# Optimization experiments

Measured on AMD Instinct MI355X. Metric: run time of the kernel, lower is better.

The kernel has to match this reference:

```python
import jax, jax.numpy as jnp
import numpy as np

TARGET_W, TARGET_H = 1024, 1024  # cv2 target_size = (width, height)
LANCZOS_A = 4  # cv2.INTER_LANCZOS4 -> 8-tap separable Lanczos, a=4


def _lanczos_matrix(n_in: int, n_out: int) -> jnp.ndarray:
    """Dense [n_out, n_in] separable Lanczos4 resampling matrix.

    OpenCV pixel-center mapping: src = (dst + 0.5) * (n_in / n_out) - 0.5,
    8 taps around floor(src), weights normalized to sum 1, replicate border.
    """
    a = LANCZOS_A
    scale = n_in / n_out
    centers = (jnp.arange(n_out, dtype=jnp.float32) + 0.5) * scale - 0.5
    base = jnp.floor(centers).astype(jnp.int32)
    taps = jnp.arange(-a + 1, a + 1, dtype=jnp.int32)          # [-3..4], 8 taps
    idx = base[:, None] + taps[None, :]                         # [n_out, 8]
    d = centers[:, None] - idx.astype(jnp.float32)
    w = jnp.sinc(d) * jnp.sinc(d / a)                           # lanczos(d)
    w = jnp.where(jnp.abs(d) < a, w, 0.0)
    w = w / jnp.sum(w, axis=1, keepdims=True)
    idx_c = jnp.clip(idx, 0, n_in - 1)                          # replicate border
    rows = jnp.broadcast_to(jnp.arange(n_out)[:, None], idx.shape)
    return jnp.zeros((n_out, n_in), dtype=jnp.float32).at[rows, idx_c].add(w)


def _resize_lanczos4(x: jnp.ndarray, out_h: int, out_w: int) -> jnp.ndarray:
    # x: [B, C, H, W] -> [B, C, out_h, out_w] via two GEMM contractions
    Wh = _lanczos_matrix(x.shape[2], out_h)
    Ww = _lanczos_matrix(x.shape[3], out_w)
    t = jnp.einsum('oh,bchw->bcow', Wh, x)   # resample height: o=out_h
    return jnp.einsum('pw,bcow->bcop', Ww, t)  # resample width: p=out_w


def _renormalize(img: jnp.ndarray) -> jnp.ndarray:
    # Per-image (over C,H,W) range renormalization, faithful to the torch loop.
    mn = jnp.min(img, axis=(1, 2, 3), keepdims=True)
    mx = jnp.max(img, axis=(1, 2, 3), keepdims=True)
    color_range = mx - mn
    ott = jnp.float32(1.0 / 255.0)    # over_top_target_range
    ubt = jnp.float32(-10.0 / 255.0)  # under_bottom_target_range
    otr = mx - 1.0                    # over_top_range
    safe_otr = jnp.where(otr != 0, otr, 1.0)
    v1 = jnp.where(img > 1,
                   (img - 1.0) * (ott / safe_otr) + (1.0 - ott),
                   jnp.where(img < 1, img * (1.0 - ott), img))
    safe_ubr = jnp.where(mn != 0, mn, 1.0)  # under_bottom_range = mn (pre-modification)
    v2 = jnp.where(v1 < 0,
                   v1 * (ubt / safe_ubr) + ubt,
                   jnp.where(v1 > 0, v1 * (1.0 - ubt), v1))
    return jnp.where(color_range > 1, v2, img)


def setup_inputs() -> dict:
    key = jax.random.key(0)
    x = jax.random.normal(key, (32, 3, 512, 512), dtype=jnp.float32)
    return {"x": x}


def reference(x):
    y = _resize_lanczos4(x, TARGET_H, TARGET_W)
    y = _renormalize(y)
    y = y * 255.0
    return y.astype(jnp.uint8)
```

## Files before the change

kernel.cpp:

```cpp
#include <hip/hip_runtime.h>

#define IN_HW 512
#define OUT_HW 1024
#define NB 32
#define NC 3
#define TOH 32
#define TOW 128
#define PATCH_H 24
#define PATCH_W 72
#define NTHREADS 256

__device__ __forceinline__ unsigned enc_f(float f) {
  unsigned u = __float_as_uint(f);
  return (u & 0x80000000u) ? ~u : (u | 0x80000000u);
}
__device__ __forceinline__ float dec_f(unsigned k) {
  unsigned u = (k & 0x80000000u) ? (k ^ 0x80000000u) : ~k;
  return __uint_as_float(u);
}

#define LW_A -0.00397053f
#define LW_B  0.03146474f
#define LW_C -0.09165979f
#define LW_D  0.28268104f
#define LW_E  0.89337959f
#define LW_F -0.15228947f
#define LW_G  0.05544842f
#define LW_H -0.01505400f

__global__ void k_init(unsigned* __restrict__ maxk, unsigned* __restrict__ mink) {
  int i = threadIdx.x;
  if (i < NB) maxk[i] = 0u;
  else if (i < 2 * NB) mink[i - NB] = 0xFFFFFFFFu;
}

__global__ __launch_bounds__(NTHREADS) void k_resize(
    const float* __restrict__ x, float* __restrict__ outf,
    unsigned* __restrict__ maxk, unsigned* __restrict__ mink) {
  __shared__ __align__(16) float patch[PATCH_H][PATCH_W];
  __shared__ float wred[8];
  const int tid = threadIdx.x;
  const int bc = blockIdx.z;
  const int oh0 = blockIdx.y * TOH, ow0 = blockIdx.x * TOW;
  const int row0 = (oh0 >> 1) - 4;
  const int col0 = (ow0 >> 1) - 4;
  const float* __restrict__ xchan = x + (size_t)bc * (IN_HW * IN_HW);

  const bool interior = (row0 >= 0) & (row0 + PATCH_H <= IN_HW) &
                        (col0 >= 0) & (col0 + PATCH_W <= IN_HW);
  if (interior) {
    for (int e = tid; e < PATCH_H * (PATCH_W / 4); e += NTHREADS) {
      int pr = e / (PATCH_W / 4), pc4 = e - pr * (PATCH_W / 4);
      const float4 v = *reinterpret_cast<const float4*>(
          xchan + (size_t)(row0 + pr) * IN_HW + (col0 + 4 * pc4));
      *reinterpret_cast<float4*>(&patch[pr][4 * pc4]) = v;
    }
  } else {
    for (int e = tid; e < PATCH_H * PATCH_W; e += NTHREADS) {
      int pr = e / PATCH_W, pc = e - pr * PATCH_W;
      int gr = row0 + pr; gr = gr < 0 ? 0 : (gr > IN_HW - 1 ? IN_HW - 1 : gr);
      int gc = col0 + pc; gc = gc < 0 ? 0 : (gc > IN_HW - 1 ? IN_HW - 1 : gc);
      patch[pr][pc] = xchan[(size_t)gr * IN_HW + gc];
    }
  }
  __syncthreads();

  const int o = tid & 15;
  const int p = tid >> 4;

  const float w0[8] = {LW_A, LW_B, LW_C, LW_D, LW_E, LW_F, LW_G, LW_H};
  const float w1[8] = {LW_H, LW_G, LW_F, LW_E, LW_D, LW_C, LW_B, LW_A};

  float ve[12], vo[12];
#pragma unroll
  for (int c = 0; c < 12; ++c) { ve[c] = 0.f; vo[c] = 0.f; }
#pragma unroll
  for (int j = 0; j < 9; ++j) {
#pragma unroll
    for (int g = 0; g < 3; ++g) {
      const float4 t = *reinterpret_cast<const float4*>(&patch[p + j][4 * (o + g)]);
      const float tv[4] = {t.x, t.y, t.z, t.w};
#pragma unroll
      for (int c = 0; c < 4; ++c) {
        if (j < 8) ve[4 * g + c] = fmaf(w0[j], tv[c], ve[4 * g + c]);
        if (j > 0) vo[4 * g + c] = fmaf(w1[j - 1], tv[c], vo[4 * g + c]);
      }
    }
  }

  float mx = -__builtin_inff(), mn = __builtin_inff();
  const size_t base = (size_t)bc * (OUT_HW * OUT_HW) +
                      (size_t)(oh0 + 2 * p) * OUT_HW + (ow0 + 8 * o);
#pragma unroll
  for (int row = 0; row < 2; ++row) {
    const float* v = row ? vo : ve;
    float px[8];
#pragma unroll
    for (int m = 0; m < 4; ++m) {
      float pe = 0.f, po = 0.f;
#pragma unroll
      for (int j = 0; j < 8; ++j) {
        pe = fmaf(w0[j], v[m + j], pe);
        po = fmaf(w1[j], v[m + 1 + j], po);
      }
      px[2 * m] = pe; px[2 * m + 1] = po;
    }
#pragma unroll
    for (int i = 0; i < 8; ++i) { mx = fmaxf(mx, px[i]); mn = fminf(mn, px[i]); }
    float* dst = outf + base + (size_t)row * OUT_HW;
    *reinterpret_cast<float4*>(dst)     = make_float4(px[0], px[1], px[2], px[3]);
    *reinterpret_cast<float4*>(dst + 4) = make_float4(px[4], px[5], px[6], px[7]);
  }

#pragma unroll
  for (int s = 32; s > 0; s >>= 1) {
    mx = fmaxf(mx, __shfl_xor(mx, s, 64));
    mn = fminf(mn, __shfl_xor(mn, s, 64));
  }
  if ((tid & 63) == 0) { wred[tid >> 6] = mx; wred[4 + (tid >> 6)] = mn; }
  __syncthreads();
  if (tid == 0) {
    float bmx = fmaxf(fmaxf(wred[0], wred[1]), fmaxf(wred[2], wred[3]));
    float bmn = fminf(fminf(wred[4], wred[5]), fminf(wred[6], wred[7]));
    int b = bc / NC;
    atomicMax(&maxk[b], enc_f(bmx));
    atomicMin(&mink[b], enc_f(bmn));
  }
}

__device__ __forceinline__ int renorm1(float img, bool applies, float cA, float cB,
                                       float om_ott, float om_ubt) {
  const float ott = 1.0f / 255.0f;
  const float ubt = -10.0f / 255.0f;
  float v1 = (img > 1.0f) ? fmaf(img - 1.0f, cA, 1.0f - ott)
           : (img < 1.0f) ? img * om_ott : img;
  float v2 = (v1 < 0.0f) ? fmaf(v1, cB, ubt)
           : (v1 > 0.0f) ? v1 * om_ubt : v1;
  float y = (applies ? v2 : img) * 255.0f;
  int t = (int)y;
  return t < 0 ? 0 : (t > 255 ? 255 : t);
}

#define N4_PER_IMG (NC * OUT_HW * OUT_HW / 4)

__global__ __launch_bounds__(NTHREADS) void k_renorm(
    int* out, const unsigned* __restrict__ maxk, const unsigned* __restrict__ mink) {
  const int b = blockIdx.y;
  const float mx = dec_f(maxk[b]);
  const float mn = dec_f(mink[b]);
  const bool applies = (mx - mn) > 1.0f;
  const float ott = 1.0f / 255.0f;
  const float ubt = -10.0f / 255.0f;
  const float otr = mx - 1.0f;
  const float cA = ott / ((otr != 0.0f) ? otr : 1.0f);
  const float cB = ubt / ((mn != 0.0f) ? mn : 1.0f);
  const float om_ott = 1.0f - ott;
  const float om_ubt = 1.0f - ubt;

  const size_t idx = (size_t)b * N4_PER_IMG +
                     (size_t)blockIdx.x * NTHREADS + threadIdx.x;
  const float4 v = reinterpret_cast<const float4*>(out)[idx];
  int4 r;
  r.x = renorm1(v.x, applies, cA, cB, om_ott, om_ubt);
  r.y = renorm1(v.y, applies, cA, cB, om_ott, om_ubt);
  r.z = renorm1(v.z, applies, cA, cB, om_ott, om_ubt);
  r.w = renorm1(v.w, applies, cA, cB, om_ott, om_ubt);
  reinterpret_cast<int4*>(out)[idx] = r;
}

extern "C" void kernel_launch(void* const* d_in, const int* in_sizes, int n_in,
                              void* d_out, int out_size, void* d_ws, size_t ws_size,
                              hipStream_t stream) {
  const float* x = (const float*)d_in[0];
  unsigned* maxk = (unsigned*)d_ws;
  unsigned* mink = maxk + NB;

  hipLaunchKernelGGL(k_init, dim3(1), dim3(64), 0, stream, maxk, mink);
  dim3 grid(OUT_HW / TOW, OUT_HW / TOH, NB * NC);
  hipLaunchKernelGGL(k_resize, grid, dim3(NTHREADS), 0, stream,
                     x, (float*)d_out, maxk, mink);
  hipLaunchKernelGGL(k_renorm, dim3(N4_PER_IMG / NTHREADS, NB), dim3(NTHREADS),
                     0, stream, (int*)d_out, maxk, mink);
}
```

Measured before the change: 815.3 us.

## Recompute Lanczos resize in two passes instead of materializing float intermediate

Splits the pipeline into a min/max pass that runs the separable Lanczos resize and only reduces per-image extrema, and a final pass that recomputes the resize and applies renormalization and quantization directly before storing. This removes the full-size float intermediate write and its read-back, at the cost of reading the input and doing the resize arithmetic twice. The shared-memory patch row is also padded from 72 to 76 floats, likely to change LDS bank mapping; this also makes the interior fast path apply to fewer tiles.

After: 855.4 us. 1.05x slower.

```diff
diff --git a/kernel.cpp b/kernel.cpp
--- a/kernel.cpp
+++ b/kernel.cpp
@@ -7,7 +7,8 @@
 #define TOH 32
 #define TOW 128
 #define PATCH_H 24
-#define PATCH_W 72
+#define PATCH_W 76
+#define PATCH_QW (PATCH_W / 4)
 #define NTHREADS 256
 
 __device__ __forceinline__ unsigned enc_f(float f) {
@@ -34,23 +35,16 @@
   else if (i < 2 * NB) mink[i - NB] = 0xFFFFFFFFu;
 }
 
-__global__ __launch_bounds__(NTHREADS) void k_resize(
-    const float* __restrict__ x, float* __restrict__ outf,
-    unsigned* __restrict__ maxk, unsigned* __restrict__ mink) {
-  __shared__ __align__(16) float patch[PATCH_H][PATCH_W];
-  __shared__ float wred[8];
-  const int tid = threadIdx.x;
-  const int bc = blockIdx.z;
-  const int oh0 = blockIdx.y * TOH, ow0 = blockIdx.x * TOW;
+__device__ __forceinline__ void lanczos_tile(
+    const float* __restrict__ xchan, int oh0, int ow0, int tid,
+    float (*patch)[PATCH_W], float pr2[2][8]) {
   const int row0 = (oh0 >> 1) - 4;
   const int col0 = (ow0 >> 1) - 4;
-  const float* __restrict__ xchan = x + (size_t)bc * (IN_HW * IN_HW);
-
   const bool interior = (row0 >= 0) & (row0 + PATCH_H <= IN_HW) &
                         (col0 >= 0) & (col0 + PATCH_W <= IN_HW);
   if (interior) {
-    for (int e = tid; e < PATCH_H * (PATCH_W / 4); e += NTHREADS) {
-      int pr = e / (PATCH_W / 4), pc4 = e - pr * (PATCH_W / 4);
+    for (int e = tid; e < PATCH_H * PATCH_QW; e += NTHREADS) {
+      int pr = e / PATCH_QW, pc4 = e - pr * PATCH_QW;
       const float4 v = *reinterpret_cast<const float4*>(
           xchan + (size_t)(row0 + pr) * IN_HW + (col0 + 4 * pc4));
       *reinterpret_cast<float4*>(&patch[pr][4 * pc4]) = v;
@@ -88,13 +82,9 @@
     }
   }
 
-  float mx = -__builtin_inff(), mn = __builtin_inff();
-  const size_t base = (size_t)bc * (OUT_HW * OUT_HW) +
-                      (size_t)(oh0 + 2 * p) * OUT_HW + (ow0 + 8 * o);
 #pragma unroll
   for (int row = 0; row < 2; ++row) {
     const float* v = row ? vo : ve;
-    float px[8];
 #pragma unroll
     for (int m = 0; m < 4; ++m) {
       float pe = 0.f, po = 0.f;
@@ -103,15 +93,29 @@
         pe = fmaf(w0[j], v[m + j], pe);
         po = fmaf(w1[j], v[m + 1 + j], po);
       }
-      px[2 * m] = pe; px[2 * m + 1] = po;
-    }
-#pragma unroll
-    for (int i = 0; i < 8; ++i) { mx = fmaxf(mx, px[i]); mn = fminf(mn, px[i]); }
-    float* dst = outf + base + (size_t)row * OUT_HW;
-    *reinterpret_cast<float4*>(dst)     = make_float4(px[0], px[1], px[2], px[3]);
-    *reinterpret_cast<float4*>(dst + 4) = make_float4(px[4], px[5], px[6], px[7]);
-  }
-
+      pr2[row][2 * m] = pe; pr2[row][2 * m + 1] = po;
+    }
+  }
+}
+
+__global__ __launch_bounds__(NTHREADS) void k_minmax(
+    const float* __restrict__ x,
+    unsigned* __restrict__ maxk, unsigned* __restrict__ mink) {
+  __shared__ __align__(16) float patch[PATCH_H][PATCH_W];
+  __shared__ float wred[8];
+  const int tid = threadIdx.x;
+  const int bc = blockIdx.z;
+  const float* __restrict__ xchan = x + (size_t)bc * (IN_HW * IN_HW);
+  float pr2[2][8];
+  lanczos_tile(xchan, blockIdx.y * TOH, blockIdx.x * TOW, tid, patch, pr2);
+
+  float mx = pr2[0][0], mn = pr2[0][0];
+#pragma unroll
+  for (int r = 0; r < 2; ++r)
+#pragma unroll
+    for (int i = 0; i < 8; ++i) {
+      mx = fmaxf(mx, pr2[r][i]); mn = fminf(mn, pr2[r][i]);
+    }
 #pragma unroll
   for (int s = 32; s > 0; s >>= 1) {
     mx = fmaxf(mx, __shfl_xor(mx, s, 64));
@@ -141,11 +145,14 @@
   return t < 0 ? 0 : (t > 255 ? 255 : t);
 }
 
-#define N4_PER_IMG (NC * OUT_HW * OUT_HW / 4)
-
-__global__ __launch_bounds__(NTHREADS) void k_renorm(
-    int* out, const unsigned* __restrict__ maxk, const unsigned* __restrict__ mink) {
-  const int b = blockIdx.y;
+__global__ __launch_bounds__(NTHREADS) void k_final(
+    const float* __restrict__ x,
+    const unsigned* __restrict__ maxk, const unsigned* __restrict__ mink,
+    int* __restrict__ out) {
+  __shared__ __align__(16) float patch[PATCH_H][PATCH_W];
+  const int tid = threadIdx.x;
+  const int bc = blockIdx.z;
+  const int b = bc / NC;
   const float mx = dec_f(maxk[b]);
   const float mn = dec_f(mink[b]);
   const bool applies = (mx - mn) > 1.0f;
@@ -157,15 +164,25 @@
   const float om_ott = 1.0f - ott;
   const float om_ubt = 1.0f - ubt;
 
-  const size_t idx = (size_t)b * N4_PER_IMG +
-                     (size_t)blockIdx.x * NTHREADS + threadIdx.x;
-  const float4 v = reinterpret_cast<const float4*>(out)[idx];
-  int4 r;
-  r.x = renorm1(v.x, applies, cA, cB, om_ott, om_ubt);
-  r.y = renorm1(v.y, applies, cA, cB, om_ott, om_ubt);
-  r.z = renorm1(v.z, applies, cA, cB, om_ott, om_ubt);
-  r.w = renorm1(v.w, applies, cA, cB, om_ott, om_ubt);
-  reinterpret_cast<int4*>(out)[idx] = r;
+  const int oh0 = blockIdx.y * TOH, ow0 = blockIdx.x * TOW;
+  const float* __restrict__ xchan = x + (size_t)bc * (IN_HW * IN_HW);
+  float pr2[2][8];
+  lanczos_tile(xchan, oh0, ow0, tid, patch, pr2);
+
+  const int o = tid & 15;
+  const int p = tid >> 4;
+  const size_t base = (size_t)bc * (OUT_HW * OUT_HW) +
+                      (size_t)(oh0 + 2 * p) * OUT_HW + (ow0 + 8 * o);
+#pragma unroll
+  for (int row = 0; row < 2; ++row) {
+    int q[8];
+#pragma unroll
+    for (int i = 0; i < 8; ++i)
+      q[i] = renorm1(pr2[row][i], applies, cA, cB, om_ott, om_ubt);
+    int* dst = out + base + (size_t)row * OUT_HW;
+    *reinterpret_cast<int4*>(dst)     = make_int4(q[0], q[1], q[2], q[3]);
+    *reinterpret_cast<int4*>(dst + 4) = make_int4(q[4], q[5], q[6], q[7]);
+  }
 }
 
 extern "C" void kernel_launch(void* const* d_in, const int* in_sizes, int n_in,
@@ -177,8 +194,7 @@
 
   hipLaunchKernelGGL(k_init, dim3(1), dim3(64), 0, stream, maxk, mink);
   dim3 grid(OUT_HW / TOW, OUT_HW / TOH, NB * NC);
-  hipLaunchKernelGGL(k_resize, grid, dim3(NTHREADS), 0, stream,
-                     x, (float*)d_out, maxk, mink);
-  hipLaunchKernelGGL(k_renorm, dim3(N4_PER_IMG / NTHREADS, NB), dim3(NTHREADS),
-                     0, stream, (int*)d_out, maxk, mink);
-}
+  hipLaunchKernelGGL(k_minmax, grid, dim3(NTHREADS), 0, stream, x, maxk, mink);
+  hipLaunchKernelGGL(k_final, grid, dim3(NTHREADS), 0, stream,
+                     x, maxk, mink, (int*)d_out);
+}
```
